# Optimization experiments

Measured on AMD Instinct MI355X. Metric: run time of the kernel, lower is better.

The kernel has to match this reference:

```python
import jax, jax.numpy as jnp
import numpy as np

B, C, H, W = 2, 256, 32, 32
NUM_HEADS = 8
HEAD_DIM = C // NUM_HEADS
SCALE = HEAD_DIM ** -0.5
K1, K2 = 2, 3
KERNELS = [3, 5, 7]
STRIDES = [1, 1, 1]
PADS = [1, 2, 3]


def avgpool2d(y, k, s, p):
    # PyTorch AvgPool2d default count_include_pad=True: divide by k*k always
    yp = jnp.pad(y, ((0, 0), (0, 0), (p, p), (p, p)))
    summed = jax.lax.reduce_window(yp, 0.0, jax.lax.add,
                                   (1, 1, k, k), (1, 1, s, s), 'VALID')
    return summed / float(k * k)


def layer_norm(x, g, b, eps=1e-5):
    mu = jnp.mean(x, axis=-1, keepdims=True)
    var = jnp.var(x, axis=-1, keepdims=True)
    return (x - mu) / jnp.sqrt(var + eps) * g + b


def topk_mask(attn, kk):
    # boolean mask with True at the top-kk positions along the last axis
    idx = jax.lax.top_k(attn, kk)[1]                     # [B,h,N,kk]
    mask = jnp.zeros(attn.shape, dtype=bool)
    return jnp.put_along_axis(mask, idx, True, axis=-1, inplace=False)


def setup_inputs() -> dict:
    key = jax.random.key(0)
    ks = jax.random.split(key, 8)
    std = 1.0 / np.sqrt(C)
    return {
        'x': jax.random.normal(ks[0], (B, C, H, W), jnp.float32),
        'y': jax.random.normal(ks[1], (B, C, H, W), jnp.float32),
        'Wq': jax.random.uniform(ks[2], (C, C), jnp.float32, -std, std),
        'Wkv': jax.random.uniform(ks[3], (2 * C, C), jnp.float32, -std, std),
        'Wproj': jax.random.uniform(ks[4], (C, C), jnp.float32, -std, std),
        'bproj': jax.random.uniform(ks[5], (C,), jnp.float32, -std, std),
        'ln_g': jnp.ones((C,), jnp.float32),
        'ln_b': jnp.zeros((C,), jnp.float32),
        'attn1_p': jnp.full((1,), 0.5, jnp.float32),
        'attn2_p': jnp.full((1,), 0.5, jnp.float32),
    }


def reference(x, y, Wq, Wkv, Wproj, bproj, ln_g, ln_b, attn1_p, attn2_p):
    # multi-scale average pooling fusion of y (stride 1 keeps H,W)
    yf = (avgpool2d(y, KERNELS[0], STRIDES[0], PADS[0])
          + avgpool2d(y, KERNELS[1], STRIDES[1], PADS[1])
          + avgpool2d(y, KERNELS[2], STRIDES[2], PADS[2]))
    yf = yf.reshape(B, C, H * W).transpose(0, 2, 1)      # [B, N1, C]
    yf = layer_norm(yf, ln_g, ln_b)
    N1 = yf.shape[1]

    kv = yf @ Wkv.T                                      # [B, N1, 2C]
    kv = kv.reshape(B, N1, 2, NUM_HEADS, HEAD_DIM).transpose(2, 0, 3, 1, 4)
    k, v = kv[0], kv[1]                                  # [B, h, N1, d]

    xf = x.reshape(B, C, H * W).transpose(0, 2, 1)       # [B, N, C]
    N = xf.shape[1]
    q = (xf @ Wq.T).reshape(B, N, NUM_HEADS, HEAD_DIM).transpose(0, 2, 1, 3)

    attn = jnp.einsum('bhnd,bhmd->bhnm', q, k) * SCALE   # [B, h, N, N1]

    neg_inf = jnp.array(-jnp.inf, attn.dtype)
    m1 = topk_mask(attn, int(N1 / K1))
    a1 = jax.nn.softmax(jnp.where(m1, attn, neg_inf), axis=-1)
    out1 = jnp.einsum('bhnm,bhmd->bhnd', a1, v)

    m2 = topk_mask(attn, int(N1 / K2))
    a2 = jax.nn.softmax(jnp.where(m2, attn, neg_inf), axis=-1)
    out2 = jnp.einsum('bhnm,bhmd->bhnd', a2, v)

    out = out1 * attn1_p + out2 * attn2_p                # [B, h, N, d]
    out = out.transpose(0, 2, 1, 3).reshape(B, N, C)
    out = out @ Wproj.T + bproj
    hw = int(np.sqrt(N))
    return out.transpose(0, 2, 1).reshape(B, C, hw, hw)
```

## Files before the change

kernel.cpp:

```cpp
#include <hip/hip_runtime.h>

typedef _Float16 f16;
typedef f16 f16x8 __attribute__((ext_vector_type(8)));
typedef float f32x4 __attribute__((ext_vector_type(4)));

constexpr float ATT_SCALE = 0.17677669529663687f;

__global__ __launch_bounds__(256) void prep_kernel(const float* __restrict__ y,
                                                   float* __restrict__ pooled,
                                                   const float* __restrict__ x,
                                                   f16* __restrict__ xT,
                                                   const float* __restrict__ Wq,
                                                   const float* __restrict__ Wkv,
                                                   const float* __restrict__ Wp,
                                                   f16* __restrict__ wq16,
                                                   f16* __restrict__ wkv16,
                                                   f16* __restrict__ wp16)
{
    __shared__ float sh[1444];
    int bid = blockIdx.x, t = threadIdx.x;
    if (bid < 512) {
        float (*p)[38] = (float(*)[38])sh;
        const float* plane = y + (size_t)bid * 1024;
        for (int i = t; i < 38 * 38; i += 256) (&p[0][0])[i] = 0.f;
        __syncthreads();
        for (int i = t; i < 1024; i += 256) p[(i >> 5) + 3][(i & 31) + 3] = plane[i];
        __syncthreads();
        for (int i = t; i < 1024; i += 256) {
            int r = (i >> 5) + 3, cc = (i & 31) + 3;
            float s3 = 0.f;
            #pragma unroll
            for (int dr = -1; dr <= 1; ++dr)
                #pragma unroll
                for (int dc = -1; dc <= 1; ++dc) s3 += p[r + dr][cc + dc];
            float r5 = 0.f;
            #pragma unroll
            for (int dc = -2; dc <= 2; ++dc) r5 += p[r - 2][cc + dc] + p[r + 2][cc + dc];
            #pragma unroll
            for (int dr = -1; dr <= 1; ++dr) r5 += p[r + dr][cc - 2] + p[r + dr][cc + 2];
            float r7 = 0.f;
            #pragma unroll
            for (int dc = -3; dc <= 3; ++dc) r7 += p[r - 3][cc + dc] + p[r + 3][cc + dc];
            #pragma unroll
            for (int dr = -2; dr <= 2; ++dr) r7 += p[r + dr][cc - 3] + p[r + dr][cc + 3];
            float s5 = s3 + r5, s7 = s5 + r7;
            pooled[(size_t)bid * 1024 + i] =
                s3 * (1.f / 9.f) + s5 * (1.f / 25.f) + s7 * (1.f / 49.f);
        }
    } else if (bid < 1024) {
        float (*tile)[33] = (float(*)[33])sh;
        int id = bid - 512;
        int b = id >> 8, ct = (id >> 5) & 7, nt = id & 31;
        int rr = t >> 5, j = t & 31;
        #pragma unroll
        for (int r = rr; r < 32; r += 8)
            tile[r][j] = x[((size_t)b * 256 + ct * 32 + r) * 1024 + nt * 32 + j];
        __syncthreads();
        #pragma unroll
        for (int r = rr; r < 32; r += 8)
            xT[((size_t)b * 1024 + nt * 32 + r) * 256 + ct * 32 + j] = (f16)tile[j][r];
    } else {
        int i = (bid - 1024) * 256 + t;
        if (i < 65536) { wq16[i] = (f16)Wq[i]; wp16[i] = (f16)Wp[i]; }
        wkv16[i] = (f16)Wkv[i];
    }
}

__global__ __launch_bounds__(256) void ln_kernel(const float* __restrict__ pooled,
                                                 const float* __restrict__ g,
                                                 const float* __restrict__ bta,
                                                 f16* __restrict__ yfln)
{
    __shared__ float tile[256][33];
    int bid = blockIdx.x;
    int b = bid >> 5, n0 = (bid & 31) * 32;
    int t = threadIdx.x;
    int cpart = t & 7;
    #pragma unroll
    for (int r0 = 0; r0 < 8; ++r0) {
        int c = r0 * 32 + (t >> 3);
        float4 v = *(const float4*)(pooled + ((size_t)b * 256 + c) * 1024 + n0 + cpart * 4);
        tile[c][cpart * 4 + 0] = v.x;
        tile[c][cpart * 4 + 1] = v.y;
        tile[c][cpart * 4 + 2] = v.z;
        tile[c][cpart * 4 + 3] = v.w;
    }
    __syncthreads();
    int w = t >> 6, lane = t & 63;
    float gg[4], bb[4];
    #pragma unroll
    for (int j = 0; j < 4; ++j) { gg[j] = g[lane + 64 * j]; bb[j] = bta[lane + 64 * j]; }
    for (int nn = 0; nn < 8; ++nn) {
        int nl = w * 8 + nn;
        float v[4];
        float s = 0.f, s2 = 0.f;
        #pragma unroll
        for (int j = 0; j < 4; ++j) {
            v[j] = tile[lane + 64 * j][nl];
            s += v[j]; s2 += v[j] * v[j];
        }
        #pragma unroll
        for (int off = 32; off; off >>= 1) { s += __shfl_xor(s, off); s2 += __shfl_xor(s2, off); }
        float mu = s * (1.f / 256.f);
        float var = s2 * (1.f / 256.f) - mu * mu;
        float rstd = rsqrtf(var + 1e-5f);
        #pragma unroll
        for (int j = 0; j < 4; ++j)
            yfln[((size_t)b * 1024 + n0 + nl) * 256 + lane + 64 * j] =
                (f16)((v[j] - mu) * rstd * gg[j] + bb[j]);
    }
}

__device__ __forceinline__ void gemm_tile(const f16* __restrict__ A, const f16* __restrict__ Bm,
                                          int row0, int ncol0, int l15, int lhi, f32x4 acc[4])
{
    for (int k0 = 0; k0 < 256; k0 += 32) {
        f16x8 a = *(const f16x8*)(A + (size_t)(row0 + l15) * 256 + k0 + lhi * 8);
        #pragma unroll
        for (int j = 0; j < 4; ++j) {
            f16x8 bf = *(const f16x8*)(Bm + (size_t)(ncol0 + j * 16 + l15) * 256 + k0 + lhi * 8);
            acc[j] = __builtin_amdgcn_mfma_f32_16x16x32_f16(a, bf, acc[j], 0, 0, 0);
        }
    }
}

__global__ __launch_bounds__(256) void qkv_kernel(const f16* __restrict__ xT,
                                                  const f16* __restrict__ yfln,
                                                  const f16* __restrict__ wq16,
                                                  const f16* __restrict__ wkv16,
                                                  f16* __restrict__ q16,
                                                  f16* __restrict__ k16,
                                                  f16* __restrict__ vT16)
{
    int w = threadIdx.x >> 6, lane = threadIdx.x & 63;
    int l15 = lane & 15, lhi = lane >> 4;
    if (blockIdx.x < 128) {
        int mt = blockIdx.x >> 2, nt = blockIdx.x & 3;
        int row0 = mt * 64 + w * 16;
        f32x4 acc[4] = {};
        gemm_tile(xT, wq16, row0, nt * 64, l15, lhi, acc);
        #pragma unroll
        for (int j = 0; j < 4; ++j) {
            int col = nt * 64 + j * 16 + l15;
            int h = col >> 5, d = col & 31;
            #pragma unroll
            for (int r = 0; r < 4; ++r) {
                int row = row0 + 4 * lhi + r;
                int b = row >> 10, n = row & 1023;
                q16[(((size_t)(b * 8 + h)) * 1024 + n) * 32 + d] = (f16)(acc[j][r] * ATT_SCALE);
            }
        }
    } else {
        int bid = blockIdx.x - 128;
        int mt = bid >> 3, nt = bid & 7;
        int row0 = mt * 64 + w * 16;
        f32x4 acc[4] = {};
        gemm_tile(yfln, wkv16, row0, nt * 64, l15, lhi, acc);
        #pragma unroll
        for (int j = 0; j < 4; ++j) {
            int col = nt * 64 + j * 16 + l15;
            #pragma unroll
            for (int r = 0; r < 4; ++r) {
                int row = row0 + 4 * lhi + r;
                int b = row >> 10, n = row & 1023;
                float v = acc[j][r];
                if (col < 256) {
                    int h = col >> 5, d = col & 31;
                    k16[(((size_t)(b * 8 + h)) * 1024 + n) * 32 + d] = (f16)v;
                } else {
                    int c2 = col - 256, h = c2 >> 5, d = c2 & 31;
                    vT16[(((size_t)(b * 8 + h)) * 32 + d) * 1024 + n] = (f16)v;
                }
            }
        }
    }
}

__global__ __launch_bounds__(1024, 8) void attn_kernel(const f16* __restrict__ q16,
                                                       const f16* __restrict__ k16,
                                                       const f16* __restrict__ vT16,
                                                       const float* __restrict__ a1p,
                                                       const float* __restrict__ a2p,
                                                       f16* __restrict__ oat)
{
    __shared__ float Sb[16 * 1024];
    __shared__ int hist[16][256];
    int bid = blockIdx.x;
    int bh = bid >> 6, rb = bid & 63;
    int row0 = rb * 16;
    int w = threadIdx.x >> 6, lane = threadIdx.x & 63;
    int l15 = lane & 15, lhi = lane >> 4;
    const f16* Qb = q16 + (size_t)bh * 32768;
    const f16* Kb = k16 + (size_t)bh * 32768;
    const f16* Vb = vT16 + (size_t)bh * 32768;

    {
        f16x8 a = *(const f16x8*)(Qb + (size_t)(row0 + l15) * 32 + lhi * 8);
        #pragma unroll
        for (int j = 0; j < 4; ++j) {
            int c0 = w * 64 + j * 16;
            f16x8 bf = *(const f16x8*)(Kb + (size_t)(c0 + l15) * 32 + lhi * 8);
            f32x4 z = {0.f, 0.f, 0.f, 0.f};
            f32x4 d = __builtin_amdgcn_mfma_f32_16x16x32_f16(a, bf, z, 0, 0, 0);
            #pragma unroll
            for (int r = 0; r < 4; ++r) {
                int rw = 4 * lhi + r;
                Sb[rw * 1024 + ((c0 + l15) ^ ((rw & 7) << 2))] = d[r];
            }
        }
    }
    #pragma unroll
    for (int i = 0; i < 4; ++i) hist[w][lane + 64 * i] = 0;
    __syncthreads();

    float c_a1 = a1p[0], c_a2 = a2p[0];
    int r = w, sw = (r & 7) << 2;
    float s[16];
    #pragma unroll
    for (int i = 0; i < 16; ++i) s[i] = Sb[r * 1024 + ((lane + 64 * i) ^ sw)];
    float mx = s[0], mn = s[0];
    #pragma unroll
    for (int i = 1; i < 16; ++i) { mx = fmaxf(mx, s[i]); mn = fminf(mn, s[i]); }
    #pragma unroll
    for (int off = 32; off; off >>= 1) {
        mx = fmaxf(mx, __shfl_xor(mx, off));
        mn = fminf(mn, __shfl_xor(mn, off));
    }
    float range = mx - mn;
    float inv = 255.0f / fmaxf(range, 1e-30f);
    #pragma unroll
    for (int i = 0; i < 16; ++i) {
        int bin = (int)((s[i] - mn) * inv);
        bin = bin < 0 ? 0 : (bin > 255 ? 255 : bin);
        atomicAdd(&hist[w][bin], 1);
    }
    int4 h4 = *(const int4*)&hist[w][lane * 4];
    int lsum = h4.x + h4.y + h4.z + h4.w;
    int acc = lsum;
    #pragma unroll
    for (int off = 1; off < 64; off <<= 1) {
        int o = __shfl_down(acc, off);
        if (lane + off < 64) acc += o;
    }
    int SA  = acc - lsum;
    int Sv3 = SA + h4.w;
    int Sv2 = Sv3 + h4.z;
    int Sv1 = Sv2 + h4.y;
    int Sv0 = Sv1 + h4.x;
    int b1l = -1, b2l = -1;
    if (Sv0 >= 512 && Sv1 < 512) b1l = 4 * lane + 0;
    if (Sv1 >= 512 && Sv2 < 512) b1l = 4 * lane + 1;
    if (Sv2 >= 512 && Sv3 < 512) b1l = 4 * lane + 2;
    if (Sv3 >= 512 && SA  < 512) b1l = 4 * lane + 3;
    if (Sv0 >= 341 && Sv1 < 341) b2l = 4 * lane + 0;
    if (Sv1 >= 341 && Sv2 < 341) b2l = 4 * lane + 1;
    if (Sv2 >= 341 && Sv3 < 341) b2l = 4 * lane + 2;
    if (Sv3 >= 341 && SA  < 341) b2l = 4 * lane + 3;
    unsigned long long mb1 = __ballot(b1l >= 0);
    int b1 = __shfl(b1l, __ffsll(mb1) - 1);
    unsigned long long mb2 = __ballot(b2l >= 0);
    int b2 = __shfl(b2l, __ffsll(mb2) - 1);

    float binw = range * (1.0f / 255.0f);
    float lo1 = mn + (float)(b1 - 1) * binw, hi1 = mn + (float)(b1 + 2) * binw;
    float lo2 = mn + (float)(b2 - 1) * binw, hi2 = mn + (float)(b2 + 2) * binw;
    bool d1 = false, d2 = false;
    for (int it = 0; it < 14; ++it) {
        if (d1 && d2) break;
        float m1 = 0.5f * (lo1 + hi1), m2 = 0.5f * (lo2 + hi2);
        if (!d1 && !(m1 > lo1 && m1 < hi1)) d1 = true;
        if (!d2 && !(m2 > lo2 && m2 < hi2)) d2 = true;
        int c1 = 0, c2 = 0;
        #pragma unroll
        for (int i = 0; i < 16; ++i) {
            c1 += (int)__popcll(__ballot(s[i] >= m1));
            c2 += (int)__popcll(__ballot(s[i] >= m2));
        }
        if (!d1) { if (c1 == 512) { d1 = true; lo1 = m1; } else if (c1 > 512) lo1 = m1; else hi1 = m1; }
        if (!d2) { if (c2 == 341) { d2 = true; lo2 = m2; } else if (c2 > 341) lo2 = m2; else hi2 = m2; }
    }
    float T1 = lo1, T2 = lo2;

    float l1 = 0.f, l2 = 0.f;
    #pragma unroll
    for (int i = 0; i < 16; ++i) {
        float e = __expf(s[i] - mx);
        if (s[i] >= T1) l1 += e;
        if (s[i] >= T2) l2 += e;
    }
    #pragma unroll
    for (int off = 32; off; off >>= 1) { l1 += __shfl_xor(l1, off); l2 += __shfl_xor(l2, off); }
    float c1 = c_a1 / l1, c2 = c_a2 / l2;
    #pragma unroll
    for (int i = 0; i < 16; ++i) {
        float e = __expf(s[i] - mx);
        float wt = (s[i] >= T1 ? c1 : 0.f) + (s[i] >= T2 ? c2 : 0.f);
        Sb[r * 1024 + ((lane + 64 * i) ^ sw)] = e * wt;
    }
    __syncthreads();

    f32x4 acc0 = {}, acc1 = {};
    int swl = (l15 & 7) << 2;
    #pragma unroll
    for (int ks = 0; ks < 2; ++ks) {
        int m0 = w * 64 + ks * 32 + lhi * 8;
        float4 ch0 = *(const float4*)&Sb[l15 * 1024 + ((m0)     ^ swl)];
        float4 ch1 = *(const float4*)&Sb[l15 * 1024 + ((m0 + 4) ^ swl)];
        f16x8 af;
        af[0] = (f16)ch0.x; af[1] = (f16)ch0.y; af[2] = (f16)ch0.z; af[3] = (f16)ch0.w;
        af[4] = (f16)ch1.x; af[5] = (f16)ch1.y; af[6] = (f16)ch1.z; af[7] = (f16)ch1.w;
        f16x8 b0 = *(const f16x8*)(Vb + (size_t)(l15) * 1024 + m0);
        f16x8 b1v = *(const f16x8*)(Vb + (size_t)(16 + l15) * 1024 + m0);
        acc0 = __builtin_amdgcn_mfma_f32_16x16x32_f16(af, b0, acc0, 0, 0, 0);
        acc1 = __builtin_amdgcn_mfma_f32_16x16x32_f16(af, b1v, acc1, 0, 0, 0);
    }
    __syncthreads();
    #pragma unroll
    for (int rr2 = 0; rr2 < 4; ++rr2) {
        int rw = 4 * lhi + rr2;
        Sb[w * 512 + rw * 32 + l15]      = acc0[rr2];
        Sb[w * 512 + rw * 32 + 16 + l15] = acc1[rr2];
    }
    __syncthreads();
    int b = bh >> 3, h = bh & 7;
    int o = threadIdx.x;
    if (o < 512) {
        int rr = o >> 5, d = o & 31;
        float v = 0.f;
        #pragma unroll
        for (int ww = 0; ww < 16; ++ww) v += Sb[ww * 512 + o];
        oat[((size_t)b * 1024 + row0 + rr) * 256 + h * 32 + d] = (f16)v;
    }
}

__global__ __launch_bounds__(256) void projgemm_kernel(const f16* __restrict__ A,
                                                       const f16* __restrict__ Bm,
                                                       const float* __restrict__ bias,
                                                       float* __restrict__ out)
{
    __shared__ float tile[64][65];
    int mt = blockIdx.x >> 2, nt = blockIdx.x & 3;
    int w = threadIdx.x >> 6, lane = threadIdx.x & 63;
    int l15 = lane & 15, lhi = lane >> 4;
    int row0 = mt * 64 + w * 16;
    f32x4 acc[4] = {};
    gemm_tile(A, Bm, row0, nt * 64, l15, lhi, acc);
    #pragma unroll
    for (int j = 0; j < 4; ++j) {
        int col_l = j * 16 + l15;
        float bv = bias[nt * 64 + col_l];
        #pragma unroll
        for (int r = 0; r < 4; ++r)
            tile[col_l][w * 16 + 4 * lhi + r] = acc[j][r] + bv;
    }
    __syncthreads();
    int b = (mt * 64) >> 10, n0 = (mt * 64) & 1023;
    int col_l = threadIdx.x >> 2, part = threadIdx.x & 3;
    size_t base = (size_t)b * 262144 + (size_t)(nt * 64 + col_l) * 1024 + n0 + part * 16;
    #pragma unroll
    for (int q = 0; q < 4; ++q) {
        float4 v;
        v.x = tile[col_l][part * 16 + q * 4 + 0];
        v.y = tile[col_l][part * 16 + q * 4 + 1];
        v.z = tile[col_l][part * 16 + q * 4 + 2];
        v.w = tile[col_l][part * 16 + q * 4 + 3];
        *(float4*)(out + base + q * 4) = v;
    }
}

extern "C" void kernel_launch(void* const* d_in, const int* in_sizes, int n_in,
                              void* d_out, int out_size, void* d_ws, size_t ws_size,
                              hipStream_t stream)
{
    const float* x     = (const float*)d_in[0];
    const float* y     = (const float*)d_in[1];
    const float* Wq    = (const float*)d_in[2];
    const float* Wkv   = (const float*)d_in[3];
    const float* Wproj = (const float*)d_in[4];
    const float* bproj = (const float*)d_in[5];
    const float* ln_g  = (const float*)d_in[6];
    const float* ln_b  = (const float*)d_in[7];
    const float* a1p   = (const float*)d_in[8];
    const float* a2p   = (const float*)d_in[9];
    float* out = (float*)d_out;

    char* wsb = (char*)d_ws;
    float* pooled = (float*)(wsb);
    f16* yfln  = (f16*)(wsb + ((size_t)2 << 20));
    f16* xT    = (f16*)(wsb + ((size_t)3 << 20));
    f16* wq16  = (f16*)(wsb + ((size_t)4 << 20));
    f16* wkv16 = (f16*)(wsb + ((size_t)4 << 20) + (128 << 10));
    f16* wp16  = (f16*)(wsb + ((size_t)4 << 20) + (384 << 10));
    f16* q16   = (f16*)(wsb + ((size_t)4 << 20) + (512 << 10));
    f16* k16   = (f16*)(wsb + ((size_t)4 << 20) + (512 << 10) + ((size_t)1 << 20));
    f16* vT16  = (f16*)(wsb + ((size_t)4 << 20) + (512 << 10) + ((size_t)2 << 20));
    f16* oat   = (f16*)(wsb + ((size_t)4 << 20) + (512 << 10) + ((size_t)3 << 20));

    prep_kernel<<<1536, 256, 0, stream>>>(y, pooled, x, xT, Wq, Wkv, Wproj,
                                          wq16, wkv16, wp16);
    ln_kernel<<<64, 256, 0, stream>>>(pooled, ln_g, ln_b, yfln);
    qkv_kernel<<<384, 256, 0, stream>>>(xT, yfln, wq16, wkv16, q16, k16, vT16);
    attn_kernel<<<1024, 1024, 0, stream>>>(q16, k16, vT16, a1p, a2p, oat);
    projgemm_kernel<<<128, 256, 0, stream>>>(oat, wp16, bproj, out);
}
```

Measured before the change: 74.34 us.

## Replace histogram top-k threshold with interpolation search and vectorize attention/LN paths

The attention kernel drops the shared-memory histogram pass. It now finds the top-k thresholds with a regula-falsi search between the row min and max, falling back to bisection every fourth step. Wave reductions use DPP instead of shuffles, score tiles are written and read as float4 by computing K·Q transposed, exponentials are cached, and the output reduction is vectorized. Pooling now writes in token-major layout so LayerNorm becomes one wave per row with vector loads across more blocks. The risk is that interpolation may need more iterations on some rows and that the strided pooled stores are uncoalesced.

New measurement: 77.90 us. 1.05x slower.

```diff
diff --git a/kernel.cpp b/kernel.cpp
--- a/kernel.cpp
+++ b/kernel.cpp
@@ -2,9 +2,35 @@
 
 typedef _Float16 f16;
 typedef f16 f16x8 __attribute__((ext_vector_type(8)));
+typedef f16 f16x4 __attribute__((ext_vector_type(4)));
 typedef float f32x4 __attribute__((ext_vector_type(4)));
 
 constexpr float ATT_SCALE = 0.17677669529663687f;
+
+template<int C> __device__ __forceinline__ float dppadd(float v) {
+    return v + __int_as_float(__builtin_amdgcn_update_dpp(0, __float_as_int(v), C, 0xf, 0xf, true));
+}
+template<int C> __device__ __forceinline__ float dppmax(float v) {
+    return fmaxf(v, __int_as_float(__builtin_amdgcn_update_dpp(__float_as_int(v), __float_as_int(v), C, 0xf, 0xf, false)));
+}
+template<int C> __device__ __forceinline__ float dppmin(float v) {
+    return fminf(v, __int_as_float(__builtin_amdgcn_update_dpp(__float_as_int(v), __float_as_int(v), C, 0xf, 0xf, false)));
+}
+__device__ __forceinline__ float wave_sum(float v) {
+    v = dppadd<0x111>(v); v = dppadd<0x112>(v); v = dppadd<0x114>(v); v = dppadd<0x118>(v);
+    v = dppadd<0x142>(v); v = dppadd<0x143>(v);
+    return __int_as_float(__builtin_amdgcn_readlane(__float_as_int(v), 63));
+}
+__device__ __forceinline__ float wave_max(float v) {
+    v = dppmax<0x111>(v); v = dppmax<0x112>(v); v = dppmax<0x114>(v); v = dppmax<0x118>(v);
+    v = dppmax<0x142>(v); v = dppmax<0x143>(v);
+    return __int_as_float(__builtin_amdgcn_readlane(__float_as_int(v), 63));
+}
+__device__ __forceinline__ float wave_min(float v) {
+    v = dppmin<0x111>(v); v = dppmin<0x112>(v); v = dppmin<0x114>(v); v = dppmin<0x118>(v);
+    v = dppmin<0x142>(v); v = dppmin<0x143>(v);
+    return __int_as_float(__builtin_amdgcn_readlane(__float_as_int(v), 63));
+}
 
 __global__ __launch_bounds__(256) void prep_kernel(const float* __restrict__ y,
                                                    float* __restrict__ pooled,
@@ -26,6 +52,7 @@
         __syncthreads();
         for (int i = t; i < 1024; i += 256) p[(i >> 5) + 3][(i & 31) + 3] = plane[i];
         __syncthreads();
+        int b = bid >> 8, c = bid & 255;
         for (int i = t; i < 1024; i += 256) {
             int r = (i >> 5) + 3, cc = (i & 31) + 3;
             float s3 = 0.f;
@@ -44,7 +71,7 @@
             #pragma unroll
             for (int dr = -2; dr <= 2; ++dr) r7 += p[r + dr][cc - 3] + p[r + dr][cc + 3];
             float s5 = s3 + r5, s7 = s5 + r7;
-            pooled[(size_t)bid * 1024 + i] =
+            pooled[((size_t)b * 1024 + i) * 256 + c] =
                 s3 * (1.f / 9.f) + s5 * (1.f / 25.f) + s7 * (1.f / 49.f);
         }
     } else if (bid < 1024) {
@@ -71,44 +98,23 @@
                                                  const float* __restrict__ bta,
                                                  f16* __restrict__ yfln)
 {
-    __shared__ float tile[256][33];
-    int bid = blockIdx.x;
-    int b = bid >> 5, n0 = (bid & 31) * 32;
-    int t = threadIdx.x;
-    int cpart = t & 7;
-    #pragma unroll
-    for (int r0 = 0; r0 < 8; ++r0) {
-        int c = r0 * 32 + (t >> 3);
-        float4 v = *(const float4*)(pooled + ((size_t)b * 256 + c) * 1024 + n0 + cpart * 4);
-        tile[c][cpart * 4 + 0] = v.x;
-        tile[c][cpart * 4 + 1] = v.y;
-        tile[c][cpart * 4 + 2] = v.z;
-        tile[c][cpart * 4 + 3] = v.w;
-    }
-    __syncthreads();
-    int w = t >> 6, lane = t & 63;
-    float gg[4], bb[4];
-    #pragma unroll
-    for (int j = 0; j < 4; ++j) { gg[j] = g[lane + 64 * j]; bb[j] = bta[lane + 64 * j]; }
-    for (int nn = 0; nn < 8; ++nn) {
-        int nl = w * 8 + nn;
-        float v[4];
-        float s = 0.f, s2 = 0.f;
-        #pragma unroll
-        for (int j = 0; j < 4; ++j) {
-            v[j] = tile[lane + 64 * j][nl];
-            s += v[j]; s2 += v[j] * v[j];
-        }
-        #pragma unroll
-        for (int off = 32; off; off >>= 1) { s += __shfl_xor(s, off); s2 += __shfl_xor(s2, off); }
-        float mu = s * (1.f / 256.f);
-        float var = s2 * (1.f / 256.f) - mu * mu;
-        float rstd = rsqrtf(var + 1e-5f);
-        #pragma unroll
-        for (int j = 0; j < 4; ++j)
-            yfln[((size_t)b * 1024 + n0 + nl) * 256 + lane + 64 * j] =
-                (f16)((v[j] - mu) * rstd * gg[j] + bb[j]);
-    }
+    int w = threadIdx.x >> 6, lane = threadIdx.x & 63;
+    int row = blockIdx.x * 4 + w;
+    float4 v = ((const float4*)(pooled + (size_t)row * 256))[lane];
+    float s  = v.x + v.y + v.z + v.w;
+    float s2 = v.x * v.x + v.y * v.y + v.z * v.z + v.w * v.w;
+    s = wave_sum(s); s2 = wave_sum(s2);
+    float mu = s * (1.f / 256.f);
+    float var = s2 * (1.f / 256.f) - mu * mu;
+    float rstd = rsqrtf(var + 1e-5f);
+    float4 gg = ((const float4*)g)[lane];
+    float4 bb = ((const float4*)bta)[lane];
+    f16x4 o;
+    o[0] = (f16)((v.x - mu) * rstd * gg.x + bb.x);
+    o[1] = (f16)((v.y - mu) * rstd * gg.y + bb.y);
+    o[2] = (f16)((v.z - mu) * rstd * gg.z + bb.z);
+    o[3] = (f16)((v.w - mu) * rstd * gg.w + bb.w);
+    *(f16x4*)(yfln + (size_t)row * 256 + lane * 4) = o;
 }
 
 __device__ __forceinline__ void gemm_tile(const f16* __restrict__ A, const f16* __restrict__ Bm,
@@ -184,7 +190,6 @@
                                                        f16* __restrict__ oat)
 {
     __shared__ float Sb[16 * 1024];
-    __shared__ int hist[16][256];
     int bid = blockIdx.x;
     int bh = bid >> 6, rb = bid & 63;
     int row0 = rb * 16;
@@ -195,107 +200,92 @@
     const f16* Vb = vT16 + (size_t)bh * 32768;
 
     {
-        f16x8 a = *(const f16x8*)(Qb + (size_t)(row0 + l15) * 32 + lhi * 8);
+        f16x8 qf = *(const f16x8*)(Qb + (size_t)(row0 + l15) * 32 + lhi * 8);
+        int q = l15, sw1 = (q & 7) << 2;
         #pragma unroll
         for (int j = 0; j < 4; ++j) {
             int c0 = w * 64 + j * 16;
-            f16x8 bf = *(const f16x8*)(Kb + (size_t)(c0 + l15) * 32 + lhi * 8);
+            f16x8 kf = *(const f16x8*)(Kb + (size_t)(c0 + l15) * 32 + lhi * 8);
             f32x4 z = {0.f, 0.f, 0.f, 0.f};
-            f32x4 d = __builtin_amdgcn_mfma_f32_16x16x32_f16(a, bf, z, 0, 0, 0);
-            #pragma unroll
-            for (int r = 0; r < 4; ++r) {
-                int rw = 4 * lhi + r;
-                Sb[rw * 1024 + ((c0 + l15) ^ ((rw & 7) << 2))] = d[r];
-            }
-        }
-    }
-    #pragma unroll
-    for (int i = 0; i < 4; ++i) hist[w][lane + 64 * i] = 0;
+            f32x4 d = __builtin_amdgcn_mfma_f32_16x16x32_f16(kf, qf, z, 0, 0, 0);
+            int k0 = c0 + 4 * lhi;
+            *(float4*)&Sb[q * 1024 + (k0 ^ sw1)] = *(float4*)&d;
+        }
+    }
     __syncthreads();
 
     float c_a1 = a1p[0], c_a2 = a2p[0];
     int r = w, sw = (r & 7) << 2;
     float s[16];
     #pragma unroll
-    for (int i = 0; i < 16; ++i) s[i] = Sb[r * 1024 + ((lane + 64 * i) ^ sw)];
-    float mx = s[0], mn = s[0];
-    #pragma unroll
-    for (int i = 1; i < 16; ++i) { mx = fmaxf(mx, s[i]); mn = fminf(mn, s[i]); }
-    #pragma unroll
-    for (int off = 32; off; off >>= 1) {
-        mx = fmaxf(mx, __shfl_xor(mx, off));
-        mn = fminf(mn, __shfl_xor(mn, off));
-    }
-    float range = mx - mn;
-    float inv = 255.0f / fmaxf(range, 1e-30f);
-    #pragma unroll
-    for (int i = 0; i < 16; ++i) {
-        int bin = (int)((s[i] - mn) * inv);
-        bin = bin < 0 ? 0 : (bin > 255 ? 255 : bin);
-        atomicAdd(&hist[w][bin], 1);
-    }
-    int4 h4 = *(const int4*)&hist[w][lane * 4];
-    int lsum = h4.x + h4.y + h4.z + h4.w;
-    int acc = lsum;
-    #pragma unroll
-    for (int off = 1; off < 64; off <<= 1) {
-        int o = __shfl_down(acc, off);
-        if (lane + off < 64) acc += o;
-    }
-    int SA  = acc - lsum;
-    int Sv3 = SA + h4.w;
-    int Sv2 = Sv3 + h4.z;
-    int Sv1 = Sv2 + h4.y;
-    int Sv0 = Sv1 + h4.x;
-    int b1l = -1, b2l = -1;
-    if (Sv0 >= 512 && Sv1 < 512) b1l = 4 * lane + 0;
-    if (Sv1 >= 512 && Sv2 < 512) b1l = 4 * lane + 1;
-    if (Sv2 >= 512 && Sv3 < 512) b1l = 4 * lane + 2;
-    if (Sv3 >= 512 && SA  < 512) b1l = 4 * lane + 3;
-    if (Sv0 >= 341 && Sv1 < 341) b2l = 4 * lane + 0;
-    if (Sv1 >= 341 && Sv2 < 341) b2l = 4 * lane + 1;
-    if (Sv2 >= 341 && Sv3 < 341) b2l = 4 * lane + 2;
-    if (Sv3 >= 341 && SA  < 341) b2l = 4 * lane + 3;
-    unsigned long long mb1 = __ballot(b1l >= 0);
-    int b1 = __shfl(b1l, __ffsll(mb1) - 1);
-    unsigned long long mb2 = __ballot(b2l >= 0);
-    int b2 = __shfl(b2l, __ffsll(mb2) - 1);
-
-    float binw = range * (1.0f / 255.0f);
-    float lo1 = mn + (float)(b1 - 1) * binw, hi1 = mn + (float)(b1 + 2) * binw;
-    float lo2 = mn + (float)(b2 - 1) * binw, hi2 = mn + (float)(b2 + 2) * binw;
-    bool d1 = false, d2 = false;
-    for (int it = 0; it < 14; ++it) {
-        if (d1 && d2) break;
-        float m1 = 0.5f * (lo1 + hi1), m2 = 0.5f * (lo2 + hi2);
-        if (!d1 && !(m1 > lo1 && m1 < hi1)) d1 = true;
-        if (!d2 && !(m2 > lo2 && m2 < hi2)) d2 = true;
+    for (int i = 0; i < 4; ++i) {
+        float4 v4 = *(const float4*)&Sb[r * 1024 + ((256 * i + 4 * lane) ^ sw)];
+        s[4 * i + 0] = v4.x; s[4 * i + 1] = v4.y; s[4 * i + 2] = v4.z; s[4 * i + 3] = v4.w;
+    }
+    float mxl = s[0], mnl = s[0];
+    #pragma unroll
+    for (int i = 1; i < 16; ++i) { mxl = fmaxf(mxl, s[i]); mnl = fminf(mnl, s[i]); }
+    float mx = wave_max(mxl), mn = wave_min(mnl);
+
+    float lo1 = mn, hi1 = mx, lo2 = mn, hi2 = mx;
+    float cl1 = 1024.f, ch1 = 1.f, cl2 = 1024.f, ch2 = 1.f;
+    bool f1 = false, f2 = false;
+    for (int it = 0; it < 16; ++it) {
+        if (f1 && f2) break;
+        float m1 = lo1, m2 = lo2;
+        bool t1 = !f1, t2 = !f2;
+        if (t1) {
+            m1 = ((it & 3) == 3) ? 0.5f * (lo1 + hi1)
+               : lo1 + (hi1 - lo1) * (cl1 - 512.f) * __builtin_amdgcn_rcpf(cl1 - ch1);
+            if (!(m1 > lo1 && m1 < hi1)) m1 = 0.5f * (lo1 + hi1);
+            if (!(m1 > lo1 && m1 < hi1)) { f1 = true; t1 = false; m1 = lo1; }
+        }
+        if (t2) {
+            m2 = ((it & 3) == 3) ? 0.5f * (lo2 + hi2)
+               : lo2 + (hi2 - lo2) * (cl2 - 341.f) * __builtin_amdgcn_rcpf(cl2 - ch2);
+            if (!(m2 > lo2 && m2 < hi2)) m2 = 0.5f * (lo2 + hi2);
+            if (!(m2 > lo2 && m2 < hi2)) { f2 = true; t2 = false; m2 = lo2; }
+        }
+        if (!t1 && !t2) break;
         int c1 = 0, c2 = 0;
         #pragma unroll
         for (int i = 0; i < 16; ++i) {
             c1 += (int)__popcll(__ballot(s[i] >= m1));
             c2 += (int)__popcll(__ballot(s[i] >= m2));
         }
-        if (!d1) { if (c1 == 512) { d1 = true; lo1 = m1; } else if (c1 > 512) lo1 = m1; else hi1 = m1; }
-        if (!d2) { if (c2 == 341) { d2 = true; lo2 = m2; } else if (c2 > 341) lo2 = m2; else hi2 = m2; }
+        if (t1) {
+            if (c1 == 512) { f1 = true; lo1 = m1; }
+            else if (c1 > 512) { lo1 = m1; cl1 = (float)c1; }
+            else { hi1 = m1; ch1 = (float)c1; }
+        }
+        if (t2) {
+            if (c2 == 341) { f2 = true; lo2 = m2; }
+            else if (c2 > 341) { lo2 = m2; cl2 = (float)c2; }
+            else { hi2 = m2; ch2 = (float)c2; }
+        }
     }
     float T1 = lo1, T2 = lo2;
 
+    float e[16];
     float l1 = 0.f, l2 = 0.f;
     #pragma unroll
     for (int i = 0; i < 16; ++i) {
-        float e = __expf(s[i] - mx);
-        if (s[i] >= T1) l1 += e;
-        if (s[i] >= T2) l2 += e;
-    }
-    #pragma unroll
-    for (int off = 32; off; off >>= 1) { l1 += __shfl_xor(l1, off); l2 += __shfl_xor(l2, off); }
-    float c1 = c_a1 / l1, c2 = c_a2 / l2;
-    #pragma unroll
-    for (int i = 0; i < 16; ++i) {
-        float e = __expf(s[i] - mx);
-        float wt = (s[i] >= T1 ? c1 : 0.f) + (s[i] >= T2 ? c2 : 0.f);
-        Sb[r * 1024 + ((lane + 64 * i) ^ sw)] = e * wt;
+        float ev = __expf(s[i] - mx);
+        e[i] = ev;
+        l1 += (s[i] >= T1) ? ev : 0.f;
+        l2 += (s[i] >= T2) ? ev : 0.f;
+    }
+    l1 = wave_sum(l1); l2 = wave_sum(l2);
+    float c1w = c_a1 / l1, c2w = c_a2 / l2;
+    #pragma unroll
+    for (int i = 0; i < 4; ++i) {
+        float4 o4;
+        float wt;
+        wt = (s[4*i+0] >= T1 ? c1w : 0.f) + (s[4*i+0] >= T2 ? c2w : 0.f); o4.x = e[4*i+0] * wt;
+        wt = (s[4*i+1] >= T1 ? c1w : 0.f) + (s[4*i+1] >= T2 ? c2w : 0.f); o4.y = e[4*i+1] * wt;
+        wt = (s[4*i+2] >= T1 ? c1w : 0.f) + (s[4*i+2] >= T2 ? c2w : 0.f); o4.z = e[4*i+2] * wt;
+        wt = (s[4*i+3] >= T1 ? c1w : 0.f) + (s[4*i+3] >= T2 ? c2w : 0.f); o4.w = e[4*i+3] * wt;
+        *(float4*)&Sb[r * 1024 + ((256 * i + 4 * lane) ^ sw)] = o4;
     }
     __syncthreads();
 
@@ -322,14 +312,19 @@
         Sb[w * 512 + rw * 32 + 16 + l15] = acc1[rr2];
     }
     __syncthreads();
-    int b = bh >> 3, h = bh & 7;
-    int o = threadIdx.x;
-    if (o < 512) {
-        int rr = o >> 5, d = o & 31;
-        float v = 0.f;
-        #pragma unroll
-        for (int ww = 0; ww < 16; ++ww) v += Sb[ww * 512 + o];
-        oat[((size_t)b * 1024 + row0 + rr) * 256 + h * 32 + d] = (f16)v;
+    if (threadIdx.x < 128) {
+        int o4 = threadIdx.x << 2;
+        float4 v = *(const float4*)&Sb[o4];
+        #pragma unroll
+        for (int ww = 1; ww < 16; ++ww) {
+            float4 p = *(const float4*)&Sb[ww * 512 + o4];
+            v.x += p.x; v.y += p.y; v.z += p.z; v.w += p.w;
+        }
+        int rr = o4 >> 5, d0 = o4 & 31;
+        int b = bh >> 3, h = bh & 7;
+        f16x4 o;
+        o[0] = (f16)v.x; o[1] = (f16)v.y; o[2] = (f16)v.z; o[3] = (f16)v.w;
+        *(f16x4*)(oat + ((size_t)b * 1024 + row0 + rr) * 256 + h * 32 + d0) = o;
     }
 }
 
@@ -398,7 +393,7 @@
 
     prep_kernel<<<1536, 256, 0, stream>>>(y, pooled, x, xT, Wq, Wkv, Wproj,
                                           wq16, wkv16, wp16);
-    ln_kernel<<<64, 256, 0, stream>>>(pooled, ln_g, ln_b, yfln);
+    ln_kernel<<<512, 256, 0, stream>>>(pooled, ln_g, ln_b, yfln);
     qkv_kernel<<<384, 256, 0, stream>>>(xT, yfln, wq16, wkv16, q16, k16, vT16);
     attn_kernel<<<1024, 1024, 0, stream>>>(q16, k16, vT16, a1p, a2p, oat);
     projgemm_kernel<<<128, 256, 0, stream>>>(oat, wp16, bproj, out);
```
